# Kernel tuning notes

Measured on AMD Instinct MI355X. Metric: run time of the kernel, lower is better.

Reference implementation:

```python
import jax, jax.numpy as jnp
import numpy as np

K_NEIGHBORS = 16


def knn_idx(x, k):
    # x: (bs, n, 3) -> (bs, n, k) indices of k nearest points (incl. self)
    sq = jnp.sum(x * x, axis=-1)                      # (bs, n)
    inner = jnp.einsum('bnd,bmd->bnm', x, x)          # (bs, n, n)
    dist = sq[:, :, None] - 2.0 * inner + sq[:, None, :]
    _, idx = jax.lax.top_k(-dist, k)
    return idx


def gather_neighbors(feat, idx):
    # feat: (bs, n, d), idx: (bs, n, k) -> (bs, n, k, d)
    bs = feat.shape[0]
    return feat[jnp.arange(bs)[:, None, None], idx]


def setup_inputs() -> dict:
    key = jax.random.key(0)
    ks = jax.random.split(key, 20)
    bs, n, emb, inner, ph, ah = 4, 2048, 128, 128, 64, 4 * 128
    s = lambda k, sh, fan: jax.random.normal(k, sh, jnp.float32) * (1.0 / np.sqrt(fan))
    return {
        'query': jax.random.normal(ks[0], (bs, n, emb), jnp.float32),
        'key': jax.random.normal(ks[1], (bs, n, emb), jnp.float32),
        'value': jax.random.normal(ks[2], (bs, n, emb), jnp.float32),
        'canonical': jax.random.normal(ks[3], (bs, n, 3), jnp.float32),
        'wq': s(ks[4], (emb, inner), emb),
        'wk': s(ks[5], (emb, inner), emb),
        'wv': s(ks[6], (emb, inner), emb),
        'wo': s(ks[7], (inner, emb), inner),
        'bo': jnp.zeros((emb,), jnp.float32),
        'p1': s(ks[8], (3, ph), 3),
        'pb1': jnp.zeros((ph,), jnp.float32),
        'p2': s(ks[9], (ph, inner), ph),
        'pb2': jnp.zeros((inner,), jnp.float32),
        'a1': s(ks[10], (inner, ah), inner),
        'ab1': jnp.zeros((ah,), jnp.float32),
        'a2': s(ks[11], (ah, inner), ah),
        'ab2': jnp.zeros((inner,), jnp.float32),
    }


def reference(query, key, value, canonical, wq, wk, wv, wo, bo,
              p1, pb1, p2, pb2, a1, ab1, a2, ab2):
    k_nb = K_NEIGHBORS
    q = query @ wq                                    # (bs, n, d)
    k = key @ wk
    v = value @ wv
    idx = knn_idx(canonical, k_nb)                    # (bs, n, k)

    pos_nn = gather_neighbors(canonical, idx)         # (bs, n, k, 3)
    rel_pos = pos_nn - canonical[:, :, None, :]
    rel_pos_emb = jax.nn.relu(rel_pos @ p1 + pb1) @ p2 + pb2  # (bs, n, k, d)

    q_nn = gather_neighbors(q, idx)
    k_nn = gather_neighbors(k, idx)
    v_nn = gather_neighbors(v, idx) + rel_pos_emb

    sim = jax.nn.relu((q_nn - k_nn + rel_pos_emb) @ a1 + ab1) @ a2 + ab2
    attn = jax.nn.softmax(sim, axis=-1)               # softmax over feature dim
    norm = jnp.maximum(jnp.linalg.norm(attn, axis=-2, keepdims=True), 1e-12)
    attn = attn / norm                                # L2-normalize over neighbors

    agg = jnp.einsum('bijd,bijd->bid', attn, v_nn)    # (bs, n, d)
    return agg @ wo + bo
```

## Files before the change

kernel.cpp:

```cpp
#include <hip/hip_runtime.h>
#include <stdint.h>

typedef unsigned short u16;
typedef unsigned int u32;
typedef unsigned long long u64;
typedef __attribute__((ext_vector_type(8))) short short8;
typedef __attribute__((ext_vector_type(4))) float f32x4;

#define BSZ 4
#define NPT 2048
#define EMB 128
#define PH  64
#define AH  512
#define KNB 16

__device__ __forceinline__ u16 f2bf(float f) {
  union { float f; u32 u; } v; v.f = f;
  u32 r = (v.u >> 16) & 1u;
  v.u += 0x7fffu + r;
  return (u16)(v.u >> 16);
}
__device__ __forceinline__ float bf2f(u16 x) {
  union { u32 u; float f; } v; v.u = ((u32)x) << 16; return v.f;
}

__global__ __launch_bounds__(256) void k_transpose(
    const float* wq, const float* wk, const float* wv, const float* p2,
    const float* a1, const float* a2, const float* wo,
    u16* wqT, u16* wkT, u16* wvT, u16* p2T, u16* a1T, u16* a2T, u16* woT) {
  const float* src; u16* dst; int K, Nn;
  switch (blockIdx.x) {
    case 0: src = wq; dst = wqT; K = 128; Nn = 128; break;
    case 1: src = wk; dst = wkT; K = 128; Nn = 128; break;
    case 2: src = wv; dst = wvT; K = 128; Nn = 128; break;
    case 3: src = p2; dst = p2T; K = 64;  Nn = 128; break;
    case 4: src = a1; dst = a1T; K = 128; Nn = 512; break;
    case 5: src = a2; dst = a2T; K = 512; Nn = 128; break;
    default: src = wo; dst = woT; K = 128; Nn = 128; break;
  }
  for (int n = threadIdx.x; n < Nn; n += 256) {
    for (int k0 = 0; k0 < K; k0 += 8) {
      short8 vv;
      #pragma unroll
      for (int t = 0; t < 8; ++t)
        vv[t] = (short)f2bf(src[(k0 + t) * Nn + n]);
      *(short8*)(dst + n * K + k0) = vv;
    }
  }
}

__device__ __forceinline__ u32 f2sort(float f) {
  union { float f; u32 u; } v; v.f = f;
  return v.u ^ ((v.u >> 31) ? 0xFFFFFFFFu : 0x80000000u);
}

__global__ __launch_bounds__(256) void k_knn(const float* __restrict__ can,
                                             int* __restrict__ idx_out) {
  __shared__ float dists[4][NPT];
  int b = blockIdx.x >> 8;
  int qblk = blockIdx.x & 255;
  const float* cb = can + (size_t)b * NPT * 3;
  int wave = threadIdx.x >> 6, lane = threadIdx.x & 63;
  float* dw = dists[wave];
  #pragma unroll 1
  for (int t = 0; t < 2; ++t) {
    int i = qblk * 8 + wave * 2 + t;
    float xi = cb[i * 3 + 0], yi = cb[i * 3 + 1], zi = cb[i * 3 + 2];
    float sqi = __fadd_rn(__fadd_rn(__fmul_rn(xi, xi), __fmul_rn(yi, yi)),
                          __fmul_rn(zi, zi));
    u64 lmin = ~0ull;
    #pragma unroll 4
    for (int c = 0; c < NPT / 64; ++c) {
      int j = c * 64 + lane;
      const float* pj = cb + j * 3;
      float xj = pj[0], yj = pj[1], zj = pj[2];
      float sqj = __fadd_rn(__fadd_rn(__fmul_rn(xj, xj), __fmul_rn(yj, yj)),
                            __fmul_rn(zj, zj));
      float nn = __fadd_rn(__fadd_rn(__fmul_rn(xi, xj), __fmul_rn(yi, yj)),
                           __fmul_rn(zi, zj));
      float dist = __fadd_rn(__fsub_rn(sqi, __fmul_rn(2.0f, nn)), sqj);
      dw[j] = dist;
      u64 key = (((u64)f2sort(dist)) << 32) | (u32)j;
      lmin = key < lmin ? key : lmin;
    }
    #pragma unroll 1
    for (int r = 0; r < KNB; ++r) {
      u64 g = lmin;
      #pragma unroll
      for (int off = 32; off > 0; off >>= 1) {
        u64 o = __shfl_xor(g, off);
        g = o < g ? o : g;
      }
      int jw = (int)(u32)(g & 0xffffffffull);
      if (lane == 0) idx_out[((size_t)b * NPT + i) * KNB + r] = jw;
      if ((jw & 63) == lane) {
        union { u32 u; float f; } inf; inf.u = 0x7f800000u;
        dw[jw] = inf.f;
        lmin = ~0ull;
        #pragma unroll
        for (int c = 0; c < NPT / 64; ++c) {
          int j = c * 64 + lane;
          u64 key = (((u64)f2sort(dw[j])) << 32) | (u32)j;
          lmin = key < lmin ? key : lmin;
        }
      }
    }
  }
}

__device__ __forceinline__ void qkv_gemm(const u16* At, const u16* wT,
                                         int colbase, int fm, int quad,
                                         f32x4 acc[2][4]) {
  #pragma unroll
  for (int tn = 0; tn < 2; ++tn)
    #pragma unroll
    for (int tm = 0; tm < 4; ++tm) acc[tn][tm] = (f32x4){0.f, 0.f, 0.f, 0.f};
  #pragma unroll
  for (int ks = 0; ks < 4; ++ks) {
    int k0 = ks * 32 + quad * 8;
    short8 bfr0 = *(const short8*)(wT + (colbase + fm) * 128 + k0);
    short8 bfr1 = *(const short8*)(wT + (colbase + 16 + fm) * 128 + k0);
    #pragma unroll
    for (int tm = 0; tm < 4; ++tm) {
      short8 afr = *(const short8*)(At + (tm * 16 + fm) * 136 + k0);
      acc[0][tm] = __builtin_amdgcn_mfma_f32_16x16x32_bf16(afr, bfr0, acc[0][tm], 0, 0, 0);
      acc[1][tm] = __builtin_amdgcn_mfma_f32_16x16x32_bf16(afr, bfr1, acc[1][tm], 0, 0, 0);
    }
  }
}

__device__ __forceinline__ void qkv_stage(u16* At, const float* src, int rbase, int tid) {
  #pragma unroll
  for (int rep = 0; rep < 4; ++rep) {
    int linear = tid + 256 * rep;
    int row = linear >> 4;
    int c16 = linear & 15;
    const float* sp = src + (size_t)(rbase + row) * 128 + c16 * 8;
    f32x4 a = *(const f32x4*)(sp);
    f32x4 b = *(const f32x4*)(sp + 4);
    short8 vv;
    vv[0] = (short)f2bf(a[0]); vv[1] = (short)f2bf(a[1]);
    vv[2] = (short)f2bf(a[2]); vv[3] = (short)f2bf(a[3]);
    vv[4] = (short)f2bf(b[0]); vv[5] = (short)f2bf(b[1]);
    vv[6] = (short)f2bf(b[2]); vv[7] = (short)f2bf(b[3]);
    *(short8*)(At + row * 136 + c16 * 8) = vv;
  }
}

__global__ __launch_bounds__(256) void k_qkv(
    const float* __restrict__ query, const float* __restrict__ key,
    const float* __restrict__ value,
    const u16* __restrict__ wqT, const u16* __restrict__ wkT,
    const u16* __restrict__ wvT,
    float* __restrict__ qk_out, float* __restrict__ v_out) {
  __shared__ __align__(16) u16 At[64 * 136];
  int tid = threadIdx.x;
  int rbase = blockIdx.x * 64;
  int lane = tid & 63, wave = tid >> 6;
  int fm = lane & 15, quad = lane >> 4;
  int colbase = wave * 32;
  f32x4 accq[2][4], acck[2][4];

  qkv_stage(At, query, rbase, tid);
  __syncthreads();
  qkv_gemm(At, wqT, colbase, fm, quad, accq);
  __syncthreads();
  qkv_stage(At, key, rbase, tid);
  __syncthreads();
  qkv_gemm(At, wkT, colbase, fm, quad, acck);
  #pragma unroll
  for (int tn = 0; tn < 2; ++tn) {
    int col = colbase + tn * 16 + fm;
    #pragma unroll
    for (int tm = 0; tm < 4; ++tm)
      #pragma unroll
      for (int r = 0; r < 4; ++r) {
        int row = tm * 16 + quad * 4 + r;
        qk_out[(size_t)(rbase + row) * 128 + col] =
            accq[tn][tm][r] - acck[tn][tm][r];
      }
  }
  __syncthreads();
  qkv_stage(At, value, rbase, tid);
  __syncthreads();
  qkv_gemm(At, wvT, colbase, fm, quad, accq);
  #pragma unroll
  for (int tn = 0; tn < 2; ++tn) {
    int col = colbase + tn * 16 + fm;
    #pragma unroll
    for (int tm = 0; tm < 4; ++tm)
      #pragma unroll
      for (int r = 0; r < 4; ++r) {
        int row = tm * 16 + quad * 4 + r;
        v_out[(size_t)(rbase + row) * 128 + col] = accq[tn][tm][r];
      }
  }
}

#define XT_LD 136
#define S_LD  132

__global__ __launch_bounds__(256) void k_attn(
    const float* __restrict__ can,
    const float* __restrict__ qk_g, const float* __restrict__ v_g,
    const int* __restrict__ idx_g,
    const float* __restrict__ p1, const float* __restrict__ pb1,
    const u16* __restrict__ p2T, const float* __restrict__ pb2,
    const u16* __restrict__ a1T, const float* __restrict__ ab1,
    const u16* __restrict__ a2T, const float* __restrict__ ab2,
    const u16* __restrict__ woT, const float* __restrict__ bo,
    float* __restrict__ out) {
  __shared__ __align__(16) char smem[53504];
  u16* Xt = (u16*)(smem);
  u16* Hs = (u16*)(smem + 17408);
  u16* R1 = (u16*)(smem + 17408);
  float* Ss = (float*)(smem);
  u16* Vn = (u16*)(smem + 34816);
  float* Agg = (float*)(smem + 51200);
  int* Idx = (int*)(smem + 53248);

  const int b = blockIdx.x >> 9;
  const int qbase = (blockIdx.x & 511) * 4;
  const int tid = threadIdx.x;
  const int lane = tid & 63, wave = tid >> 6;
  const int fm = lane & 15, quad = lane >> 4;
  const int colbase = wave * 32;

  if (tid < 64) Idx[tid] = idx_g[((size_t)b * NPT + qbase) * KNB + tid];
  __syncthreads();

  {
    int row = tid >> 2, part = tid & 3;
    int j = Idx[row];
    int qi = qbase + (row >> 4);
    const float* cb = can + (size_t)b * NPT * 3;
    float r0 = cb[j * 3 + 0] - cb[qi * 3 + 0];
    float r1 = cb[j * 3 + 1] - cb[qi * 3 + 1];
    float r2 = cb[j * 3 + 2] - cb[qi * 3 + 2];
    int h0 = part * 16;
    #pragma unroll
    for (int hp = 0; hp < 8; ++hp) {
      u32 pack = 0;
      #pragma unroll
      for (int e = 0; e < 2; ++e) {
        int hh = h0 + hp * 2 + e;
        float s = r0 * p1[hh];
        s = fmaf(r1, p1[PH + hh], s);
        s = fmaf(r2, p1[2 * PH + hh], s);
        s += pb1[hh];
        s = fmaxf(s, 0.0f);
        pack |= ((u32)f2bf(s)) << (16 * e);
      }
      *(u32*)(R1 + row * 72 + h0 + hp * 2) = pack;
    }
  }
  __syncthreads();

  {
    f32x4 acc[2][4];
    #pragma unroll
    for (int tn = 0; tn < 2; ++tn)
      #pragma unroll
      for (int tm = 0; tm < 4; ++tm) acc[tn][tm] = (f32x4){0.f, 0.f, 0.f, 0.f};
    #pragma unroll
    for (int ks = 0; ks < 2; ++ks) {
      int k0 = ks * 32 + quad * 8;
      short8 bfr0 = *(const short8*)(p2T + (colbase + fm) * PH + k0);
      short8 bfr1 = *(const short8*)(p2T + (colbase + 16 + fm) * PH + k0);
      #pragma unroll
      for (int tm = 0; tm < 4; ++tm) {
        short8 afr = *(const short8*)(R1 + (tm * 16 + fm) * 72 + k0);
        acc[0][tm] = __builtin_amdgcn_mfma_f32_16x16x32_bf16(afr, bfr0, acc[0][tm], 0, 0, 0);
        acc[1][tm] = __builtin_amdgcn_mfma_f32_16x16x32_bf16(afr, bfr1, acc[1][tm], 0, 0, 0);
      }
    }
    #pragma unroll
    for (int tn = 0; tn < 2; ++tn) {
      int col = colbase + tn * 16 + fm;
      float pb2c = pb2[col];
      #pragma unroll
      for (int tm = 0; tm < 4; ++tm)
        #pragma unroll
        for (int r = 0; r < 4; ++r) {
          int row = tm * 16 + quad * 4 + r;
          int j = Idx[row];
          float rpe = acc[tn][tm][r] + pb2c;
          size_t base = ((size_t)b * NPT + j) * EMB + col;
          Xt[row * XT_LD + col] = f2bf(qk_g[base] + rpe);
          Vn[row * 128 + col] = f2bf(v_g[base] + rpe);
        }
    }
  }
  __syncthreads();

  f32x4 accS[2][4];
  #pragma unroll
  for (int tn = 0; tn < 2; ++tn)
    #pragma unroll
    for (int tm = 0; tm < 4; ++tm) accS[tn][tm] = (f32x4){0.f, 0.f, 0.f, 0.f};
  #pragma unroll 1
  for (int c = 0; c < 4; ++c) {
    f32x4 acc1[2][4];
    #pragma unroll
    for (int tn = 0; tn < 2; ++tn)
      #pragma unroll
      for (int tm = 0; tm < 4; ++tm) acc1[tn][tm] = (f32x4){0.f, 0.f, 0.f, 0.f};
    #pragma unroll
    for (int ks = 0; ks < 4; ++ks) {
      int k0 = ks * 32 + quad * 8;
      short8 bfr0 = *(const short8*)(a1T + (c * 128 + colbase + fm) * 128 + k0);
      short8 bfr1 = *(const short8*)(a1T + (c * 128 + colbase + 16 + fm) * 128 + k0);
      #pragma unroll
      for (int tm = 0; tm < 4; ++tm) {
        short8 afr = *(const short8*)(Xt + (tm * 16 + fm) * XT_LD + k0);
        acc1[0][tm] = __builtin_amdgcn_mfma_f32_16x16x32_bf16(afr, bfr0, acc1[0][tm], 0, 0, 0);
        acc1[1][tm] = __builtin_amdgcn_mfma_f32_16x16x32_bf16(afr, bfr1, acc1[1][tm], 0, 0, 0);
      }
    }
    #pragma unroll
    for (int tn = 0; tn < 2; ++tn) {
      int lcol = colbase + tn * 16 + fm;
      float ab1c = ab1[c * 128 + lcol];
      #pragma unroll
      for (int tm = 0; tm < 4; ++tm)
        #pragma unroll
        for (int r = 0; r < 4; ++r) {
          int row = tm * 16 + quad * 4 + r;
          Hs[row * XT_LD + lcol] = f2bf(fmaxf(acc1[tn][tm][r] + ab1c, 0.0f));
        }
    }
    __syncthreads();
    #pragma unroll
    for (int ks = 0; ks < 4; ++ks) {
      int k0 = ks * 32 + quad * 8;
      short8 bfr0 = *(const short8*)(a2T + (colbase + fm) * AH + c * 128 + k0);
      short8 bfr1 = *(const short8*)(a2T + (colbase + 16 + fm) * AH + c * 128 + k0);
      #pragma unroll
      for (int tm = 0; tm < 4; ++tm) {
        short8 afr = *(const short8*)(Hs + (tm * 16 + fm) * XT_LD + k0);
        accS[0][tm] = __builtin_amdgcn_mfma_f32_16x16x32_bf16(afr, bfr0, accS[0][tm], 0, 0, 0);
        accS[1][tm] = __builtin_amdgcn_mfma_f32_16x16x32_bf16(afr, bfr1, accS[1][tm], 0, 0, 0);
      }
    }
    __syncthreads();
  }

  #pragma unroll
  for (int tn = 0; tn < 2; ++tn) {
    int col = colbase + tn * 16 + fm;
    float ab2c = ab2[col];
    #pragma unroll
    for (int tm = 0; tm < 4; ++tm)
      #pragma unroll
      for (int r = 0; r < 4; ++r) {
        int row = tm * 16 + quad * 4 + r;
        Ss[row * S_LD + col] = accS[tn][tm][r] + ab2c;
      }
  }
  __syncthreads();

  {
    int row = tid >> 2, part = tid & 3;
    float* srow = Ss + row * S_LD + part * 32;
    float ev[32];
    float m = -3.0e38f;
    #pragma unroll
    for (int c2 = 0; c2 < 32; ++c2) { ev[c2] = srow[c2]; m = fmaxf(m, ev[c2]); }
    m = fmaxf(m, __shfl_xor(m, 1));
    m = fmaxf(m, __shfl_xor(m, 2));
    float sum = 0.f;
    #pragma unroll
    for (int c2 = 0; c2 < 32; ++c2) { ev[c2] = __expf(ev[c2] - m); sum += ev[c2]; }
    sum += __shfl_xor(sum, 1);
    sum += __shfl_xor(sum, 2);
    float inv = 1.0f / sum;
    #pragma unroll
    for (int c2 = 0; c2 < 32; ++c2) srow[c2] = ev[c2] * inv;
  }
  __syncthreads();

  #pragma unroll
  for (int u = 0; u < 2; ++u) {
    int cid = tid + 256 * u;
    int q = cid >> 7, d = cid & 127;
    float ss = 0.f, av = 0.f;
    #pragma unroll
    for (int jj = 0; jj < 16; ++jj) {
      float a = Ss[(q * 16 + jj) * S_LD + d];
      ss = fmaf(a, a, ss);
      av = fmaf(a, bf2f(Vn[(q * 16 + jj) * 128 + d]), av);
    }
    float nrm = fmaxf(sqrtf(ss), 1e-12f);
    Agg[q * EMB + d] = av / nrm;
  }
  __syncthreads();

  {
    int d = tid & 127, qp = tid >> 7;
    float boc = bo[d];
    #pragma unroll
    for (int qi2 = 0; qi2 < 2; ++qi2) {
      int q = qp * 2 + qi2;
      float o = 0.f;
      #pragma unroll
      for (int k8 = 0; k8 < 16; ++k8) {
        short8 w8 = *(const short8*)(woT + d * 128 + k8 * 8);
        #pragma unroll
        for (int e = 0; e < 8; ++e)
          o = fmaf(Agg[q * EMB + k8 * 8 + e], bf2f((u16)w8[e]), o);
      }
      out[((size_t)b * NPT + qbase + q) * EMB + d] = o + boc;
    }
  }
}

extern "C" void kernel_launch(void* const* d_in, const int* in_sizes, int n_in,
                              void* d_out, int out_size, void* d_ws, size_t ws_size,
                              hipStream_t stream) {
  (void)in_sizes; (void)n_in; (void)out_size; (void)ws_size;
  const float* query = (const float*)d_in[0];
  const float* key_i = (const float*)d_in[1];
  const float* value = (const float*)d_in[2];
  const float* can   = (const float*)d_in[3];
  const float* wq  = (const float*)d_in[4];
  const float* wk  = (const float*)d_in[5];
  const float* wv  = (const float*)d_in[6];
  const float* wo  = (const float*)d_in[7];
  const float* bo  = (const float*)d_in[8];
  const float* p1  = (const float*)d_in[9];
  const float* pb1 = (const float*)d_in[10];
  const float* p2  = (const float*)d_in[11];
  const float* pb2 = (const float*)d_in[12];
  const float* a1  = (const float*)d_in[13];
  const float* ab1 = (const float*)d_in[14];
  const float* a2  = (const float*)d_in[15];
  const float* ab2 = (const float*)d_in[16];

  char* ws = (char*)d_ws;
  float* qk_ws = (float*)(ws + 0);
  float* v_ws  = (float*)(ws + 4194304);
  int* idx_ws  = (int*)(ws + 8388608);
  u16* wqT = (u16*)(ws + 8912896);
  u16* wkT = (u16*)(ws + 8945664);
  u16* wvT = (u16*)(ws + 8978432);
  u16* p2T = (u16*)(ws + 9011200);
  u16* a1T = (u16*)(ws + 9027584);
  u16* a2T = (u16*)(ws + 9158656);
  u16* woT = (u16*)(ws + 9289728);
  float* out = (float*)d_out;

  k_transpose<<<dim3(7), dim3(256), 0, stream>>>(
      wq, wk, wv, p2, a1, a2, wo, wqT, wkT, wvT, p2T, a1T, a2T, woT);
  k_knn<<<dim3(1024), dim3(256), 0, stream>>>(can, idx_ws);
  k_qkv<<<dim3(128), dim3(256), 0, stream>>>(
      query, key_i, value, wqT, wkT, wvT, qk_ws, v_ws);
  k_attn<<<dim3(2048), dim3(256), 0, stream>>>(
      can, qk_ws, v_ws, idx_ws, p1, pb1, p2T, pb2, a1T, ab1, a2T, ab2,
      woT, bo, out);
}
```

Before: 315.5 us.

## Keep softmax and neighbor aggregation in MFMA registers, shrink LDS footprint

The softmax over features, the L2 norm over neighbors and the weighted aggregation now run directly on the MFMA accumulator registers. Row max and sum use cross-lane shuffles plus a small LDS reduction across waves instead of spilling the full score matrix to shared memory. The neighbor values are kept packed as bf16 in registers rather than stored in an LDS tile. This cuts LDS use from about 53KB to 39KB, and the launch bounds are set to request 4 blocks per CU for higher occupancy. The cost is more register pressure and extra shuffle work, and the R1 write pattern is also interleaved.

```diff
diff --git a/kernel.cpp b/kernel.cpp
--- a/kernel.cpp
+++ b/kernel.cpp
@@ -198,9 +198,8 @@
 }
 
 #define XT_LD 136
-#define S_LD  132
-
-__global__ __launch_bounds__(256) void k_attn(
+
+__global__ __launch_bounds__(256, 4) void k_attn(
     const float* __restrict__ can,
     const float* __restrict__ qk_g, const float* __restrict__ v_g,
     const int* __restrict__ idx_g,
@@ -210,14 +209,14 @@
     const u16* __restrict__ a2T, const float* __restrict__ ab2,
     const u16* __restrict__ woT, const float* __restrict__ bo,
     float* __restrict__ out) {
-  __shared__ __align__(16) char smem[53504];
+  __shared__ __align__(16) char smem[39168];
   u16* Xt = (u16*)(smem);
   u16* Hs = (u16*)(smem + 17408);
   u16* R1 = (u16*)(smem + 17408);
-  float* Ss = (float*)(smem);
-  u16* Vn = (u16*)(smem + 34816);
-  float* Agg = (float*)(smem + 51200);
-  int* Idx = (int*)(smem + 53248);
+  float* Red1 = (float*)(smem + 34816);
+  float* Red2 = (float*)(smem + 35840);
+  float* Agg = (float*)(smem + 36864);
+  int* Idx = (int*)(smem + 38912);
 
   const int b = blockIdx.x >> 9;
   const int qbase = (blockIdx.x & 511) * 4;
@@ -237,13 +236,13 @@
     float r0 = cb[j * 3 + 0] - cb[qi * 3 + 0];
     float r1 = cb[j * 3 + 1] - cb[qi * 3 + 1];
     float r2 = cb[j * 3 + 2] - cb[qi * 3 + 2];
-    int h0 = part * 16;
     #pragma unroll
     for (int hp = 0; hp < 8; ++hp) {
+      int cp = part + 4 * hp;
       u32 pack = 0;
       #pragma unroll
       for (int e = 0; e < 2; ++e) {
-        int hh = h0 + hp * 2 + e;
+        int hh = cp * 2 + e;
         float s = r0 * p1[hh];
         s = fmaf(r1, p1[PH + hh], s);
         s = fmaf(r2, p1[2 * PH + hh], s);
@@ -251,11 +250,12 @@
         s = fmaxf(s, 0.0f);
         pack |= ((u32)f2bf(s)) << (16 * e);
       }
-      *(u32*)(R1 + row * 72 + h0 + hp * 2) = pack;
-    }
-  }
-  __syncthreads();
-
+      *(u32*)(R1 + row * 72 + cp * 2) = pack;
+    }
+  }
+  __syncthreads();
+
+  u32 vp[4][4];
   {
     f32x4 acc[2][4];
     #pragma unroll
@@ -287,7 +287,8 @@
           float rpe = acc[tn][tm][r] + pb2c;
           size_t base = ((size_t)b * NPT + j) * EMB + col;
           Xt[row * XT_LD + col] = f2bf(qk_g[base] + rpe);
-          Vn[row * 128 + col] = f2bf(v_g[base] + rpe);
+          u32 vb = (u32)f2bf(v_g[base] + rpe);
+          if (tn == 0) vp[tm][r] = vb; else vp[tm][r] |= vb << 16;
         }
     }
   }
@@ -345,54 +346,92 @@
     __syncthreads();
   }
 
-  #pragma unroll
-  for (int tn = 0; tn < 2; ++tn) {
-    int col = colbase + tn * 16 + fm;
-    float ab2c = ab2[col];
+  {
+    float ab2c0 = ab2[colbase + fm];
+    float ab2c1 = ab2[colbase + 16 + fm];
+    float rm[4][4];
     #pragma unroll
     for (int tm = 0; tm < 4; ++tm)
       #pragma unroll
       for (int r = 0; r < 4; ++r) {
+        accS[0][tm][r] += ab2c0;
+        accS[1][tm][r] += ab2c1;
+        rm[tm][r] = fmaxf(accS[0][tm][r], accS[1][tm][r]);
+      }
+    #pragma unroll
+    for (int off = 1; off <= 8; off <<= 1)
+      #pragma unroll
+      for (int tm = 0; tm < 4; ++tm)
+        #pragma unroll
+        for (int r = 0; r < 4; ++r)
+          rm[tm][r] = fmaxf(rm[tm][r], __shfl_xor(rm[tm][r], off));
+    if (fm == 0) {
+      #pragma unroll
+      for (int tm = 0; tm < 4; ++tm)
+        #pragma unroll
+        for (int r = 0; r < 4; ++r)
+          Red1[wave * 64 + tm * 16 + quad * 4 + r] = rm[tm][r];
+    }
+    __syncthreads();
+    #pragma unroll
+    for (int tm = 0; tm < 4; ++tm)
+      #pragma unroll
+      for (int r = 0; r < 4; ++r) {
         int row = tm * 16 + quad * 4 + r;
-        Ss[row * S_LD + col] = accS[tn][tm][r] + ab2c;
-      }
-  }
-  __syncthreads();
-
-  {
-    int row = tid >> 2, part = tid & 3;
-    float* srow = Ss + row * S_LD + part * 32;
-    float ev[32];
-    float m = -3.0e38f;
-    #pragma unroll
-    for (int c2 = 0; c2 < 32; ++c2) { ev[c2] = srow[c2]; m = fmaxf(m, ev[c2]); }
-    m = fmaxf(m, __shfl_xor(m, 1));
-    m = fmaxf(m, __shfl_xor(m, 2));
-    float sum = 0.f;
-    #pragma unroll
-    for (int c2 = 0; c2 < 32; ++c2) { ev[c2] = __expf(ev[c2] - m); sum += ev[c2]; }
-    sum += __shfl_xor(sum, 1);
-    sum += __shfl_xor(sum, 2);
-    float inv = 1.0f / sum;
-    #pragma unroll
-    for (int c2 = 0; c2 < 32; ++c2) srow[c2] = ev[c2] * inv;
-  }
-  __syncthreads();
-
-  #pragma unroll
-  for (int u = 0; u < 2; ++u) {
-    int cid = tid + 256 * u;
-    int q = cid >> 7, d = cid & 127;
-    float ss = 0.f, av = 0.f;
-    #pragma unroll
-    for (int jj = 0; jj < 16; ++jj) {
-      float a = Ss[(q * 16 + jj) * S_LD + d];
-      ss = fmaf(a, a, ss);
-      av = fmaf(a, bf2f(Vn[(q * 16 + jj) * 128 + d]), av);
-    }
-    float nrm = fmaxf(sqrtf(ss), 1e-12f);
-    Agg[q * EMB + d] = av / nrm;
-  }
+        float m = fmaxf(fmaxf(Red1[row], Red1[64 + row]),
+                        fmaxf(Red1[128 + row], Red1[192 + row]));
+        float e0 = __expf(accS[0][tm][r] - m);
+        float e1 = __expf(accS[1][tm][r] - m);
+        accS[0][tm][r] = e0;
+        accS[1][tm][r] = e1;
+        rm[tm][r] = e0 + e1;
+      }
+    #pragma unroll
+    for (int off = 1; off <= 8; off <<= 1)
+      #pragma unroll
+      for (int tm = 0; tm < 4; ++tm)
+        #pragma unroll
+        for (int r = 0; r < 4; ++r)
+          rm[tm][r] += __shfl_xor(rm[tm][r], off);
+    if (fm == 0) {
+      #pragma unroll
+      for (int tm = 0; tm < 4; ++tm)
+        #pragma unroll
+        for (int r = 0; r < 4; ++r)
+          Red2[wave * 64 + tm * 16 + quad * 4 + r] = rm[tm][r];
+    }
+    __syncthreads();
+    #pragma unroll
+    for (int tm = 0; tm < 4; ++tm)
+      #pragma unroll
+      for (int r = 0; r < 4; ++r) {
+        int row = tm * 16 + quad * 4 + r;
+        float sum = (Red2[row] + Red2[64 + row]) +
+                    (Red2[128 + row] + Red2[192 + row]);
+        float inv = 1.0f / sum;
+        accS[0][tm][r] *= inv;
+        accS[1][tm][r] *= inv;
+      }
+  }
+
+  #pragma unroll
+  for (int tn = 0; tn < 2; ++tn)
+    #pragma unroll
+    for (int tm = 0; tm < 4; ++tm) {
+      float ssq = 0.f, wav = 0.f;
+      #pragma unroll
+      for (int r = 0; r < 4; ++r) {
+        float a = accS[tn][tm][r];
+        u16 vb = (u16)(tn == 0 ? (vp[tm][r] & 0xffffu) : (vp[tm][r] >> 16));
+        ssq = fmaf(a, a, ssq);
+        wav = fmaf(a, bf2f(vb), wav);
+      }
+      ssq += __shfl_xor(ssq, 16); ssq += __shfl_xor(ssq, 32);
+      wav += __shfl_xor(wav, 16); wav += __shfl_xor(wav, 32);
+      if (quad == 0)
+        Agg[tm * EMB + colbase + tn * 16 + fm] =
+            wav / fmaxf(sqrtf(ssq), 1e-12f);
+    }
   __syncthreads();
 
   {
```

Measured after the change: 340.8 us. 8.0% more time.
